# Kernel optimization log

Hardware: AMD Instinct MI355X
Metric: run time of the kernel (lower is better)

Reference implementation:

```python
import jax, jax.numpy as jnp
import numpy as np

D = 128
N = 20000
E = 60000
L = 5  # levels 0..4; level 0 = primary inputs
PER = N // L
# processing order in the original forward: AND(3), NOT(2), XOR(5), MAJ(1), OR(4)
CODES = [3, 2, 5, 1, 4]
FIDX = {3: 0, 5: 1, 1: 2, 4: 3}  # index into 2D-input func aggregators


def _gru(x, h, wih, whh, bih, bhh):
    # single-step torch.nn.GRU cell. wih:[D,3D], whh:[D,3D]
    gi = x @ wih + bih
    gh = h @ whh + bhh
    ir, iz, inn = jnp.split(gi, 3, axis=-1)
    hr, hz, hn = jnp.split(gh, 3, axis=-1)
    r = jax.nn.sigmoid(ir + hr)
    z = jax.nn.sigmoid(iz + hz)
    n = jnp.tanh(inn + r * hn)
    return (1.0 - z) * n + z * h


def setup_inputs() -> dict:
    rng = np.random.default_rng(0)
    # topological levels, contiguous blocks of PER nodes per level
    forward_level = np.repeat(np.arange(L), PER).astype(np.int32)
    gate = np.zeros(N, dtype=np.int32)
    gate[PER:] = rng.integers(1, 6, size=N - PER)  # gates 1..5 for non-PI nodes
    # DAG edges: dst at level>=1, src strictly below dst's level
    dst = rng.integers(PER, N, size=E)
    dst_level = forward_level[dst].astype(np.int64)
    src = (rng.random(E) * (dst_level * PER)).astype(np.int64)
    edge_index = np.stack([src, dst]).astype(np.int32)

    key = jax.random.key(0)
    ks = iter(jax.random.split(key, 64))
    s = 0.08
    p = {}
    p['hs_init'] = jax.random.normal(next(ks), (N, D), jnp.float32)
    # strc aggregators (5 gate types, input D): 2-layer MLP
    p['Ws1'] = jax.random.normal(next(ks), (5, D, D)) * s
    p['bs1'] = jnp.zeros((5, D))
    p['Ws2'] = jax.random.normal(next(ks), (5, D, D)) * s
    p['bs2'] = jnp.zeros((5, D))
    # func aggregators with 2D input (and, xor, maj, or)
    p['Wf1'] = jax.random.normal(next(ks), (4, 2 * D, D)) * s
    p['bf1'] = jnp.zeros((4, D))
    p['Wf2'] = jax.random.normal(next(ks), (4, D, D)) * s
    p['bf2'] = jnp.zeros((4, D))
    # not_func aggregator (input D)
    p['Wnf1'] = jax.random.normal(next(ks), (D, D)) * s
    p['bnf1'] = jnp.zeros((D,))
    p['Wnf2'] = jax.random.normal(next(ks), (D, D)) * s
    p['bnf2'] = jnp.zeros((D,))
    # GRU params, stacked over 5 gate types, strc and func
    for pre in ('Gs', 'Gf'):
        p[pre + '_wih'] = jax.random.normal(next(ks), (5, D, 3 * D)) * s
        p[pre + '_whh'] = jax.random.normal(next(ks), (5, D, 3 * D)) * s
        p[pre + '_bih'] = jnp.zeros((5, 3 * D))
        p[pre + '_bhh'] = jnp.zeros((5, 3 * D))
    p['edge_index'] = jnp.asarray(edge_index)
    p['gate'] = jnp.asarray(gate)
    p['forward_level'] = jnp.asarray(forward_level)
    p['num_levels'] = L
    return p


def reference(hs_init, Ws1, bs1, Ws2, bs2, Wf1, bf1, Wf2, bf2,
              Wnf1, bnf1, Wnf2, bnf2,
              Gs_wih, Gs_whh, Gs_bih, Gs_bhh,
              Gf_wih, Gf_whh, Gf_bih, Gf_bhh,
              edge_index, gate, forward_level, num_levels):
    src, dst = edge_index[0], edge_index[1]
    pi_mask = (gate == 0)
    hs = jnp.where(pi_mask[:, None], hs_init, 0.0)  # generate_hs_init: encode PIs
    hf = jnp.zeros_like(hs)
    node_state = jnp.concatenate([hs, hf], axis=-1)

    for level in range(1, num_levels):
        for t, code in enumerate(CODES):
            nmask = (forward_level == level) & (gate == code)  # [N]
            emask = nmask[dst].astype(hs.dtype)[:, None]       # edges into these nodes
            # --- structural message: MLP(hs[src]) summed into dst
            m = jax.nn.relu(hs[src] @ Ws1[t] + bs1[t]) @ Ws2[t] + bs2[t]
            agg = jax.ops.segment_sum(m * emask, dst, num_segments=N)
            h_new = _gru(agg, hs, Gs_wih[t], Gs_whh[t], Gs_bih[t], Gs_bhh[t])
            hs = jnp.where(nmask[:, None], h_new, hs)
            # --- functional message
            if code == 2:  # NOT uses current hf only
                m = jax.nn.relu(hf[src] @ Wnf1 + bnf1) @ Wnf2 + bnf2
            else:
                fi = FIDX[code]
                m = jax.nn.relu(node_state[src] @ Wf1[fi] + bf1[fi]) @ Wf2[fi] + bf2[fi]
            agg = jax.ops.segment_sum(m * emask, dst, num_segments=N)
            h_new = _gru(agg, hf, Gf_wih[t], Gf_whh[t], Gf_bih[t], Gf_bhh[t])
            hf = jnp.where(nmask[:, None], h_new, hf)
        node_state = jnp.concatenate([hs, hf], axis=-1)
    return hs, hf
```

## Files before the change

kernel.cpp:

```cpp
#include <hip/hip_runtime.h>
#include <hip/hip_bf16.h>

typedef __hip_bfloat16 bf16;
typedef unsigned short ushortT;
typedef __attribute__((ext_vector_type(8))) short bf16x8;
typedef __attribute__((ext_vector_type(4))) float f32x4;

#define D 128
#define NLEV 5
#define TE 16
#define TN 16

#define OFF_S1 0
#define OFF_S2 81920
#define OFF_F1 163840
#define OFF_F2 294912
#define OFF_NF1 360448
#define OFF_NF2 376832
#define WT_TOTAL 393216

__constant__ int TMAP[6] = { -1, 3, 1, 0, 4, 2 };
__constant__ int FMAP[6] = { -1, 2, -1, 0, 3, 1 };

__device__ int g_flag;

__device__ __forceinline__ float sigm(float x) { return 1.0f / (1.0f + __expf(-x)); }

__device__ __forceinline__ float rlane(float v, int ln) {
    return __int_as_float(__builtin_amdgcn_readlane(__float_as_int(v), ln));
}

__device__ __forceinline__ ushortT f2b(float v) {
    bf16 h = __float2bfloat16(v);
    return *reinterpret_cast<ushortT*>(&h);
}

template <int ISB>
__device__ __forceinline__ float ld(const void* p, size_t i) {
    if (ISB) return __bfloat162float(((const bf16*)p)[i]);
    return ((const float*)p)[i];
}

template <int ISB>
__device__ __forceinline__ float2 ld2(const void* p, size_t i) {
    if (ISB) {
        __hip_bfloat162 v = *(const __hip_bfloat162*)((const bf16*)p + i);
        return make_float2(__bfloat162float(v.x), __bfloat162float(v.y));
    }
    return *(const float2*)((const float*)p + i);
}

__global__ void detect_dtype(const void* hs_init) {
    int t = threadIdx.x;
    float x = __bfloat162float(((const bf16*)hs_init)[2 * t]);
    float ax = fabsf(x);
    bool sane = (x == 0.0f) || (ax > 1e-4f && ax < 64.0f);
    unsigned long long m = __ballot(sane);
    if (t == 0) g_flag = (__popcll(m) >= 32) ? 1 : 0;
}

__global__ void init_state(const void* __restrict__ hs_init,
                           const int* __restrict__ gate,
                           float* __restrict__ hs, float* __restrict__ hf,
                           ushortT* __restrict__ hsb, ushortT* __restrict__ hfb) {
    int v = blockIdx.x;
    int j = threadIdx.x;
    size_t idx = (size_t)v * D + j;
    bool pi = (gate[v] == 0);
    float val = 0.f;
    ushortT bval = 0;
    if (pi) {
        if (g_flag) {
            bval = ((const ushortT*)hs_init)[idx];
            bf16 h = *reinterpret_cast<bf16*>(&bval);
            val = __bfloat162float(h);
        } else {
            val = ((const float*)hs_init)[idx];
            bval = f2b(val);
        }
    }
    hs[idx] = val; hf[idx] = 0.f;
    hsb[idx] = bval; hfb[idx] = 0;
}

__global__ void transpose_w(const void* __restrict__ src, ushortT* __restrict__ dst,
                            int K, int C) {
    int n = blockIdx.y, c = blockIdx.x;
    ushortT* d = dst + (size_t)n * C * K;
    if (g_flag) {
        const ushortT* s = (const ushortT*)src + (size_t)n * K * C;
        for (int k = threadIdx.x; k < K; k += blockDim.x)
            d[(size_t)c * K + k] = s[(size_t)k * C + c];
    } else {
        const float* s = (const float*)src + (size_t)n * K * C;
        for (int k = threadIdx.x; k < K; k += blockDim.x)
            d[(size_t)c * K + k] = f2b(s[(size_t)k * C + c]);
    }
}

__global__ void count_bins(const int* __restrict__ dstA, const int* __restrict__ gate,
                           const int* __restrict__ lev, int E, int N,
                           int* __restrict__ ecnt, int* __restrict__ ncnt,
                           int* __restrict__ ndeg) {
    __shared__ int lc[40];
    int tid = threadIdx.x;
    if (tid < 40) lc[tid] = 0;
    __syncthreads();
    int i = blockIdx.x * blockDim.x + tid;
    if (i < E) {
        int d = dstA[i]; int l = lev[d];
        if (l >= 1 && l < NLEV) {
            atomicAdd(&lc[(l - 1) * 5 + TMAP[gate[d]]], 1);
            atomicAdd(&ndeg[d], 1);
        }
    }
    if (i < N) {
        int l = lev[i];
        if (l >= 1 && l < NLEV && gate[i] >= 1) atomicAdd(&lc[20 + (l - 1) * 5 + TMAP[gate[i]]], 1);
    }
    __syncthreads();
    if (tid < 20 && lc[tid]) atomicAdd(&ecnt[tid], lc[tid]);
    if (tid >= 20 && tid < 40 && lc[tid]) atomicAdd(&ncnt[tid - 20], lc[tid]);
}

__global__ void scan_offsets(const int* __restrict__ ecnt, const int* __restrict__ ncnt,
                             int* __restrict__ eoff, int* __restrict__ noff) {
    if (threadIdx.x == 0 && blockIdx.x == 0) {
        int o = 0;
        for (int b = 0; b < 20; ++b) { eoff[b] = o; o += ((ecnt[b] + TE - 1) / TE) * TE; }
        eoff[20] = o;
        o = 0;
        for (int b = 0; b < 20; ++b) { noff[b] = o; o += ((ncnt[b] + TN - 1) / TN) * TN; }
        noff[20] = o;
    }
}

__global__ void fill_bins(const int* __restrict__ gate, const int* __restrict__ lev, int N,
                          const int* __restrict__ noff, int* __restrict__ ncur,
                          int* __restrict__ nlist) {
    __shared__ int nc[20], nb[20];
    int tid = threadIdx.x;
    if (tid < 20) nc[tid] = 0;
    __syncthreads();
    int i = blockIdx.x * blockDim.x + tid;
    int bn = -1, rn = 0;
    if (i < N) {
        int l = lev[i];
        if (l >= 1 && l < NLEV && gate[i] >= 1) { bn = (l - 1) * 5 + TMAP[gate[i]]; rn = atomicAdd(&nc[bn], 1); }
    }
    __syncthreads();
    if (tid < 20) nb[tid] = nc[tid] ? atomicAdd(&ncur[tid], nc[tid]) : 0;
    __syncthreads();
    if (bn >= 0) nlist[noff[bn] + nb[bn] + rn] = i;
}

__global__ __launch_bounds__(256) void bucket_scan(
    const int* __restrict__ nlist, const int* __restrict__ noff,
    const int* __restrict__ ncnt, const int* __restrict__ eoff,
    const int* __restrict__ ndeg, int* __restrict__ nodeoff) {
    int b = blockIdx.x;
    int start = noff[b];
    int cnt = ncnt[b];
    int ebase = eoff[b];
    __shared__ int sc[256];
    int tid = threadIdx.x;
    int carry = 0;
    for (int chunk = 0; chunk < cnt; chunk += 256) {
        __syncthreads();
        int i = chunk + tid;
        int v = -1, dg = 0;
        if (i < cnt) { v = nlist[start + i]; dg = ndeg[v]; }
        sc[tid] = dg;
        __syncthreads();
        for (int off = 1; off < 256; off <<= 1) {
            int y = (tid >= off) ? sc[tid - off] : 0;
            __syncthreads();
            sc[tid] += y;
            __syncthreads();
        }
        if (v >= 0) nodeoff[v] = ebase + carry + (sc[tid] - dg);
        carry += sc[255];
    }
}

__global__ void fill_edges(const int* __restrict__ dstA, const int* __restrict__ lev,
                           int E, const int* __restrict__ nodeoff,
                           int* __restrict__ ecur_n, int* __restrict__ elist) {
    int i = blockIdx.x * blockDim.x + threadIdx.x;
    if (i >= E) return;
    int d = dstA[i];
    int l = lev[d];
    if (l >= 1 && l < NLEV) {
        int pos = nodeoff[d] + atomicAdd(&ecur_n[d], 1);
        elist[pos] = i;
    }
}

__global__ __launch_bounds__(256) void edge_mfma(
    const ushortT* __restrict__ hsb, const ushortT* __restrict__ hfb,
    const ushortT* __restrict__ wt,
    const void* __restrict__ bs1, const void* __restrict__ bs2,
    const void* __restrict__ bf1, const void* __restrict__ bf2,
    const void* __restrict__ bnf1, const void* __restrict__ bnf2,
    const int* __restrict__ dstA, const int* __restrict__ srcA,
    const int* __restrict__ gate,
    const int* __restrict__ eoff, const int* __restrict__ elist,
    float* __restrict__ agg_s, float* __restrict__ agg_f, int level) {
    int lo = eoff[(level - 1) * 5];
    int hi = eoff[(level - 1) * 5 + 5];
    int base = lo + blockIdx.x * TE;
    if (base >= hi) return;

    __shared__ int se[TE], de[TE];
    __shared__ bf16 hid[2][16][136];
    __shared__ float emsg[2][16][128];

    int tid = threadIdx.x;
    int wv = tid >> 6, pass = wv >> 1, hc = wv & 1, l = tid & 63;
    int lg = l >> 4, lr = l & 15;
    int isb = g_flag;

    int c = gate[dstA[elist[base]]];
    int t = TMAP[c], fi = FMAP[c];

    if (tid < TE) {
        int e = elist[base + tid];
        se[tid] = (e < 0) ? -1 : srcA[e];
        de[tid] = (e < 0) ? -1 : dstA[e];
    }
    __syncthreads();

    int src = se[lr];

    int KS1; size_t wb1; int K1;
    if (pass == 0)      { KS1 = 4; wb1 = OFF_S1 + (size_t)t * 16384; K1 = 128; }
    else if (c == 2)    { KS1 = 4; wb1 = OFF_NF1; K1 = 128; }
    else                { KS1 = 8; wb1 = OFF_F1 + (size_t)fi * 32768; K1 = 256; }

    f32x4 a0 = {0.f,0.f,0.f,0.f}, a1 = a0, a2 = a0, a3 = a0;
    for (int ks = 0; ks < KS1; ++ks) {
        bf16x8 a = {0,0,0,0,0,0,0,0};
        if (src >= 0) {
            int kk = ks * 32 + lg * 8;
            const ushortT* ap;
            if (pass == 0)      ap = hsb + (size_t)src * D + kk;
            else if (c == 2)    ap = hfb + (size_t)src * D + kk;
            else                ap = (kk < 128) ? (hsb + (size_t)src * D + kk)
                                                : (hfb + (size_t)src * D + (kk - 128));
            a = *(const bf16x8*)ap;
        }
        int kb = ks * 32 + lg * 8;
        {
            bf16x8 b = *(const bf16x8*)&wt[wb1 + (size_t)(hc * 64 + 0 * 16 + lr) * K1 + kb];
            a0 = __builtin_amdgcn_mfma_f32_16x16x32_bf16(a, b, a0, 0, 0, 0);
        }
        {
            bf16x8 b = *(const bf16x8*)&wt[wb1 + (size_t)(hc * 64 + 1 * 16 + lr) * K1 + kb];
            a1 = __builtin_amdgcn_mfma_f32_16x16x32_bf16(a, b, a1, 0, 0, 0);
        }
        {
            bf16x8 b = *(const bf16x8*)&wt[wb1 + (size_t)(hc * 64 + 2 * 16 + lr) * K1 + kb];
            a2 = __builtin_amdgcn_mfma_f32_16x16x32_bf16(a, b, a2, 0, 0, 0);
        }
        {
            bf16x8 b = *(const bf16x8*)&wt[wb1 + (size_t)(hc * 64 + 3 * 16 + lr) * K1 + kb];
            a3 = __builtin_amdgcn_mfma_f32_16x16x32_bf16(a, b, a3, 0, 0, 0);
        }
    }

    const void* b1p = (pass == 0) ? bs1 : (c == 2 ? bnf1 : bf1);
    size_t b1o = (pass == 0) ? (size_t)t * D : (c == 2 ? 0 : (size_t)fi * D);
    {
        f32x4 av[4] = { a0, a1, a2, a3 };
#pragma unroll
        for (int ct = 0; ct < 4; ++ct) {
            int cc = hc * 64 + ct * 16 + lr;
            float bb = isb ? ld<1>(b1p, b1o + cc) : ld<0>(b1p, b1o + cc);
#pragma unroll
            for (int r = 0; r < 4; ++r) {
                int m = lg * 4 + r;
                float v = fmaxf(av[ct][r] + bb, 0.f);
                hid[pass][m][cc] = __float2bfloat16(v);
            }
        }
    }
    __syncthreads();

    size_t wb2 = (pass == 0) ? (OFF_S2 + (size_t)t * 16384)
                             : (c == 2 ? (size_t)OFF_NF2 : (OFF_F2 + (size_t)fi * 16384));
    a0 = (f32x4){0.f,0.f,0.f,0.f}; a1 = a0; a2 = a0; a3 = a0;
#pragma unroll
    for (int ks = 0; ks < 4; ++ks) {
        bf16x8 a = *(const bf16x8*)&hid[pass][lr][ks * 32 + lg * 8];
        int kb = ks * 32 + lg * 8;
        {
            bf16x8 b = *(const bf16x8*)&wt[wb2 + (size_t)(hc * 64 + 0 * 16 + lr) * 128 + kb];
            a0 = __builtin_amdgcn_mfma_f32_16x16x32_bf16(a, b, a0, 0, 0, 0);
        }
        {
            bf16x8 b = *(const bf16x8*)&wt[wb2 + (size_t)(hc * 64 + 1 * 16 + lr) * 128 + kb];
            a1 = __builtin_amdgcn_mfma_f32_16x16x32_bf16(a, b, a1, 0, 0, 0);
        }
        {
            bf16x8 b = *(const bf16x8*)&wt[wb2 + (size_t)(hc * 64 + 2 * 16 + lr) * 128 + kb];
            a2 = __builtin_amdgcn_mfma_f32_16x16x32_bf16(a, b, a2, 0, 0, 0);
        }
        {
            bf16x8 b = *(const bf16x8*)&wt[wb2 + (size_t)(hc * 64 + 3 * 16 + lr) * 128 + kb];
            a3 = __builtin_amdgcn_mfma_f32_16x16x32_bf16(a, b, a3, 0, 0, 0);
        }
    }

    const void* b2p = (pass == 0) ? bs2 : (c == 2 ? bnf2 : bf2);
    size_t b2o = (pass == 0) ? (size_t)t * D : (c == 2 ? 0 : (size_t)fi * D);
    {
        f32x4 av[4] = { a0, a1, a2, a3 };
#pragma unroll
        for (int ct = 0; ct < 4; ++ct) {
            int cc = hc * 64 + ct * 16 + lr;
            float bb = isb ? ld<1>(b2p, b2o + cc) : ld<0>(b2p, b2o + cc);
#pragma unroll
            for (int r = 0; r < 4; ++r) {
                int m = lg * 4 + r;
                emsg[pass][m][cc] = av[ct][r] + bb;
            }
        }
    }
    __syncthreads();

    float* aggp = pass ? agg_f : agg_s;
    int col = hc * 64 + l;
    float s = 0.f;
    for (int m = 0; m < TE; ++m) {
        int d = de[m];
        if (d < 0) break;
        s += emsg[pass][m][col];
        bool flush = (m == TE - 1) || (de[m + 1] != d);
        if (flush) {
            atomicAdd(&aggp[(size_t)d * D + col], s);
            s = 0.f;
        }
    }
}

template <int ISB, int MC, int R>
__device__ __forceinline__ void mmB(
    const float (&x0)[R], const float (&x1)[R],
    const void* __restrict__ W, size_t wofs, int wstride,
    int mstart, int c0, float (&out)[R][2]) {
#pragma unroll 4
    for (int mm = 0; mm < MC; ++mm) {
        int m = mstart + mm;
        float2 w0 = ld2<ISB>(W, wofs + (size_t)(2 * m) * wstride + c0);
        float2 w1 = ld2<ISB>(W, wofs + (size_t)(2 * m + 1) * wstride + c0);
#pragma unroll
        for (int r = 0; r < R; ++r) {
            float xa = rlane(x0[r], m);
            float xb = rlane(x1[r], m);
            out[r][0] = fmaf(xb, w1.x, fmaf(xa, w0.x, out[r][0]));
            out[r][1] = fmaf(xb, w1.y, fmaf(xa, w0.y, out[r][1]));
        }
    }
}

template <int ISB>
__device__ void node_fused_body(
    const float* __restrict__ agg_s, const float* __restrict__ agg_f,
    const void* __restrict__ Gs_wih, const void* __restrict__ Gf_wih,
    const void* __restrict__ Gs_bih, const void* __restrict__ Gs_bhh,
    const void* __restrict__ Gf_bih, const void* __restrict__ Gf_bhh,
    float* __restrict__ hs, float* __restrict__ hf,
    ushortT* __restrict__ hsb, ushortT* __restrict__ hfb,
    const int* __restrict__ gate,
    const int* __restrict__ noff, const int* __restrict__ nlist,
    int level, float (*gi)[3][16][128]) {
    int lo = noff[(level - 1) * 5];
    int hi = noff[(level - 1) * 5 + 5];
    int base = lo + blockIdx.x * TN;
    if (base >= hi) return;
    int tid = threadIdx.x;
    int w = tid >> 6, l = tid & 63;
    int p = w / 6, r6 = w % 6, gg = r6 >> 1, rh = r6 & 1;
    int c0 = 2 * l;
    int t = TMAP[gate[nlist[base]]];

    const float* agg = p ? agg_f : agg_s;
    const void* wih = p ? Gf_wih : Gs_wih;

    float x0[8], x1[8];
#pragma unroll
    for (int r = 0; r < 8; ++r) {
        int v = nlist[base + rh * 8 + r];
        float2 a = (v >= 0) ? *(const float2*)&agg[(size_t)v * D + c0]
                            : make_float2(0.f, 0.f);
        x0[r] = a.x; x1[r] = a.y;
    }
    float acc[8][2];
#pragma unroll
    for (int r = 0; r < 8; ++r) { acc[r][0] = 0.f; acc[r][1] = 0.f; }
    mmB<ISB, 64, 8>(x0, x1, wih, (size_t)t * D * 3 * D, 3 * D, 0, gg * 128 + c0, acc);
#pragma unroll
    for (int r = 0; r < 8; ++r) {
        gi[p][gg][rh * 8 + r][c0] = acc[r][0];
        gi[p][gg][rh * 8 + r][c0 + 1] = acc[r][1];
    }
    __syncthreads();

    if (tid < 256) {
        int pp = tid >> 7, j = tid & 127;
        const void* bih = pp ? Gf_bih : Gs_bih;
        const void* bhh = pp ? Gf_bhh : Gs_bhh;
        float br = ld<ISB>(bih, (size_t)t * 384 + j);
        float bz = ld<ISB>(bih, (size_t)t * 384 + 128 + j);
        float bn = ld<ISB>(bih, (size_t)t * 384 + 256 + j);
        float hr = ld<ISB>(bhh, (size_t)t * 384 + j);
        float hz = ld<ISB>(bhh, (size_t)t * 384 + 128 + j);
        float hn = ld<ISB>(bhh, (size_t)t * 384 + 256 + j);
        float* ho = pp ? hf : hs;
        ushortT* hb = pp ? hfb : hsb;
#pragma unroll
        for (int r = 0; r < TN; ++r) {
            int v = nlist[base + r];
            if (v < 0) continue;
            float rr = sigm(gi[pp][0][r][j] + br + hr);
            float z = sigm(gi[pp][1][r][j] + bz + hz);
            float n = tanhf(gi[pp][2][r][j] + bn + rr * hn);
            float out = (1.f - z) * n;
            ho[(size_t)v * D + j] = out;
            hb[(size_t)v * D + j] = f2b(out);
        }
    }
}

__global__ __launch_bounds__(768) void node_fused(
    const float* agg_s, const float* agg_f,
    const void* Gs_wih, const void* Gf_wih,
    const void* Gs_bih, const void* Gs_bhh,
    const void* Gf_bih, const void* Gf_bhh,
    float* hs, float* hf, ushortT* hsb, ushortT* hfb,
    const int* gate, const int* noff, const int* nlist, int level) {
    __shared__ float gi[2][3][16][128];
    if (g_flag)
        node_fused_body<1>(agg_s, agg_f, Gs_wih, Gf_wih, Gs_bih, Gs_bhh,
                           Gf_bih, Gf_bhh, hs, hf, hsb, hfb, gate, noff, nlist,
                           level, gi);
    else
        node_fused_body<0>(agg_s, agg_f, Gs_wih, Gf_wih, Gs_bih, Gs_bhh,
                           Gf_bih, Gf_bhh, hs, hf, hsb, hfb, gate, noff, nlist,
                           level, gi);
}

__global__ void writeout(const float* __restrict__ hs, const float* __restrict__ hf,
                         void* __restrict__ out, int ND) {
    int i = blockIdx.x * blockDim.x + threadIdx.x;
    if (i >= ND) return;
    if (g_flag) {
        ((ushortT*)out)[i] = f2b(hs[i]);
        ((ushortT*)out)[ND + i] = f2b(hf[i]);
    } else {
        ((float*)out)[i] = hs[i];
        ((float*)out)[ND + i] = hf[i];
    }
}

extern "C" void kernel_launch(void* const* d_in, const int* in_sizes, int n_in,
                              void* d_out, int out_size, void* d_ws, size_t ws_size,
                              hipStream_t stream) {
    const void* hs_init = d_in[0];
    const void* Ws1 = d_in[1];
    const void* bs1 = d_in[2];
    const void* Ws2 = d_in[3];
    const void* bs2 = d_in[4];
    const void* Wf1 = d_in[5];
    const void* bf1 = d_in[6];
    const void* Wf2 = d_in[7];
    const void* bf2 = d_in[8];
    const void* Wnf1 = d_in[9];
    const void* bnf1 = d_in[10];
    const void* Wnf2 = d_in[11];
    const void* bnf2 = d_in[12];
    const void* Gs_wih = d_in[13];
    const void* Gs_bih = d_in[15];
    const void* Gs_bhh = d_in[16];
    const void* Gf_wih = d_in[17];
    const void* Gf_bih = d_in[19];
    const void* Gf_bhh = d_in[20];
    const int* edge_index = (const int*)d_in[21];
    const int* gate = (const int*)d_in[22];
    const int* lev = (const int*)d_in[23];

    int E = in_sizes[21] / 2;
    int N = in_sizes[22];
    int ND = N * D;
    int cap = ((N / NLEV + 5 * TN + 64) + TN - 1) / TN * TN;

    float* hs = (float*)d_ws;
    float* hf = hs + ND;
    float* agg_s = hf + ND;
    float* agg_f = agg_s + ND;
    ushortT* hsb = (ushortT*)(agg_f + ND);
    ushortT* hfb = hsb + ND;
    ushortT* wt = hfb + ND;
    int* meta = (int*)(wt + WT_TOTAL);
    int* ecnt = meta;
    int* ncnt = ecnt + 20;
    int* ncur = ncnt + 20;
    int* eoff = ncur + 20;
    int* noff = eoff + 21;
    int* ndeg = meta + 128;
    int* ecur_n = ndeg + N;
    int* nodeoff = ecur_n + N;
    int* elist = nodeoff + N;
    int* nlist = elist + (E + 20 * TE);

    const int* srcA = edge_index;
    const int* dstA = edge_index + E;

    detect_dtype<<<1, 64, 0, stream>>>(hs_init);
    hipMemsetAsync(agg_s, 0, (size_t)2 * ND * sizeof(float), stream);
    hipMemsetAsync(meta, 0, (size_t)(128 + 2 * N) * sizeof(int), stream);
    hipMemsetAsync(elist, 0xFF, (size_t)(E + 20 * TE + N + 20 * TN) * sizeof(int), stream);
    init_state<<<N, D, 0, stream>>>(hs_init, gate, hs, hf, hsb, hfb);

    transpose_w<<<dim3(128, 5), 128, 0, stream>>>(Ws1, wt + OFF_S1, 128, 128);
    transpose_w<<<dim3(128, 5), 128, 0, stream>>>(Ws2, wt + OFF_S2, 128, 128);
    transpose_w<<<dim3(128, 4), 256, 0, stream>>>(Wf1, wt + OFF_F1, 256, 128);
    transpose_w<<<dim3(128, 4), 128, 0, stream>>>(Wf2, wt + OFF_F2, 128, 128);
    transpose_w<<<dim3(128, 1), 128, 0, stream>>>(Wnf1, wt + OFF_NF1, 128, 128);
    transpose_w<<<dim3(128, 1), 128, 0, stream>>>(Wnf2, wt + OFF_NF2, 128, 128);

    int mx = (E > N) ? E : N;
    count_bins<<<(mx + 255) / 256, 256, 0, stream>>>(dstA, gate, lev, E, N, ecnt, ncnt, ndeg);
    scan_offsets<<<1, 64, 0, stream>>>(ecnt, ncnt, eoff, noff);
    fill_bins<<<(N + 255) / 256, 256, 0, stream>>>(gate, lev, N, noff, ncur, nlist);
    bucket_scan<<<20, 256, 0, stream>>>(nlist, noff, ncnt, eoff, ndeg, nodeoff);
    fill_edges<<<(E + 255) / 256, 256, 0, stream>>>(dstA, lev, E, nodeoff, ecur_n, elist);

    int gridE = (E + 20 * TE) / TE + 1;
    int gridNcap = cap / TN;
    for (int level = 1; level < NLEV; ++level) {
        edge_mfma<<<gridE, 256, 0, stream>>>(hsb, hfb, wt,
                                             bs1, bs2, bf1, bf2, bnf1, bnf2,
                                             dstA, srcA, gate, eoff, elist,
                                             agg_s, agg_f, level);
        node_fused<<<gridNcap, 768, 0, stream>>>(agg_s, agg_f, Gs_wih, Gf_wih,
                                                 Gs_bih, Gs_bhh, Gf_bih, Gf_bhh,
                                                 hs, hf, hsb, hfb,
                                                 gate, noff, nlist, level);
    }

    writeout<<<(ND + 255) / 256, 256, 0, stream>>>(hs, hf, d_out, ND);
}
```

Baseline: 302.2 us.

## Use split-bf16 MFMA for node GRU input projection with pretransposed weights

Replaces the scalar readlane/FMA matmul for the GRU input projection in node_fused with bf16 MFMA 16x16x32 instructions. To keep accuracy close to fp32, activations are split into hi and lo bf16 parts, and for fp32 inputs the weights get a lo residual too (three MFMAs per tile). GRU weights are pretransposed to bf16 hi/lo buffers in a single merged prep_weights kernel that replaces six transpose launches. This adds workspace and extra MFMA passes, and the split-bf16 scheme is not exactly equal to fp32 accumulation.

```diff
diff --git a/kernel.cpp b/kernel.cpp
--- a/kernel.cpp
+++ b/kernel.cpp
@@ -17,7 +17,11 @@
 #define OFF_F2 294912
 #define OFF_NF1 360448
 #define OFF_NF2 376832
-#define WT_TOTAL 393216
+#define OFF_GSH 393216
+#define OFF_GFH 638976
+#define OFF_GSL 884736
+#define OFF_GFL 1130496
+#define WT_TOTAL 1376256
 
 __constant__ int TMAP[6] = { -1, 3, 1, 0, 4, 2 };
 __constant__ int FMAP[6] = { -1, 2, -1, 0, 3, 1 };
@@ -25,10 +29,6 @@
 __device__ int g_flag;
 
 __device__ __forceinline__ float sigm(float x) { return 1.0f / (1.0f + __expf(-x)); }
-
-__device__ __forceinline__ float rlane(float v, int ln) {
-    return __int_as_float(__builtin_amdgcn_readlane(__float_as_int(v), ln));
-}
 
 __device__ __forceinline__ ushortT f2b(float v) {
     bf16 h = __float2bfloat16(v);
@@ -39,15 +39,6 @@
 __device__ __forceinline__ float ld(const void* p, size_t i) {
     if (ISB) return __bfloat162float(((const bf16*)p)[i]);
     return ((const float*)p)[i];
-}
-
-template <int ISB>
-__device__ __forceinline__ float2 ld2(const void* p, size_t i) {
-    if (ISB) {
-        __hip_bfloat162 v = *(const __hip_bfloat162*)((const bf16*)p + i);
-        return make_float2(__bfloat162float(v.x), __bfloat162float(v.y));
-    }
-    return *(const float2*)((const float*)p + i);
 }
 
 __global__ void detect_dtype(const void* hs_init) {
@@ -83,19 +74,38 @@
     hsb[idx] = bval; hfb[idx] = 0;
 }
 
-__global__ void transpose_w(const void* __restrict__ src, ushortT* __restrict__ dst,
-                            int K, int C) {
-    int n = blockIdx.y, c = blockIdx.x;
-    ushortT* d = dst + (size_t)n * C * K;
-    if (g_flag) {
-        const ushortT* s = (const ushortT*)src + (size_t)n * K * C;
-        for (int k = threadIdx.x; k < K; k += blockDim.x)
-            d[(size_t)c * K + k] = s[(size_t)k * C + c];
+__global__ void prep_weights(const void* __restrict__ Ws1, const void* __restrict__ Ws2,
+                             const void* __restrict__ Wf1, const void* __restrict__ Wf2,
+                             const void* __restrict__ Wnf1, const void* __restrict__ Wnf2,
+                             const void* __restrict__ Gs, const void* __restrict__ Gf,
+                             ushortT* __restrict__ wt) {
+    int i = blockIdx.x * blockDim.x + threadIdx.x;
+    if (i >= WT_TOTAL) return;
+    const void* src; int Kd, C, rem, mode = 0;
+    if (i < OFF_S2)       { src = Ws1;  rem = i;           Kd = 128; C = 128; }
+    else if (i < OFF_F1)  { src = Ws2;  rem = i - OFF_S2;  Kd = 128; C = 128; }
+    else if (i < OFF_F2)  { src = Wf1;  rem = i - OFF_F1;  Kd = 256; C = 128; }
+    else if (i < OFF_NF1) { src = Wf2;  rem = i - OFF_F2;  Kd = 128; C = 128; }
+    else if (i < OFF_NF2) { src = Wnf1; rem = i - OFF_NF1; Kd = 128; C = 128; }
+    else if (i < OFF_GSH) { src = Wnf2; rem = i - OFF_NF2; Kd = 128; C = 128; }
+    else if (i < OFF_GFH) { src = Gs;   rem = i - OFF_GSH; Kd = 128; C = 384; mode = 1; }
+    else if (i < OFF_GSL) { src = Gf;   rem = i - OFF_GFH; Kd = 128; C = 384; mode = 1; }
+    else if (i < OFF_GFL) { src = Gs;   rem = i - OFF_GSL; Kd = 128; C = 384; mode = 2; }
+    else                  { src = Gf;   rem = i - OFF_GFL; Kd = 128; C = 384; mode = 2; }
+    int n = rem / (Kd * C);
+    int r2 = rem % (Kd * C);
+    int c = r2 / Kd;
+    int k = r2 % Kd;
+    size_t si = (size_t)n * Kd * C + (size_t)k * C + c;
+    float v = g_flag ? ld<1>(src, si) : ld<0>(src, si);
+    ushortT out;
+    if (mode == 2) {
+        bf16 h = __float2bfloat16(v);
+        out = f2b(v - __bfloat162float(h));
     } else {
-        const float* s = (const float*)src + (size_t)n * K * C;
-        for (int k = threadIdx.x; k < K; k += blockDim.x)
-            d[(size_t)c * K + k] = f2b(s[(size_t)k * C + c]);
-    }
+        out = f2b(v);
+    }
+    wt[i] = out;
 }
 
 __global__ void count_bins(const int* __restrict__ dstA, const int* __restrict__ gate,
@@ -343,30 +353,10 @@
     }
 }
 
-template <int ISB, int MC, int R>
-__device__ __forceinline__ void mmB(
-    const float (&x0)[R], const float (&x1)[R],
-    const void* __restrict__ W, size_t wofs, int wstride,
-    int mstart, int c0, float (&out)[R][2]) {
-#pragma unroll 4
-    for (int mm = 0; mm < MC; ++mm) {
-        int m = mstart + mm;
-        float2 w0 = ld2<ISB>(W, wofs + (size_t)(2 * m) * wstride + c0);
-        float2 w1 = ld2<ISB>(W, wofs + (size_t)(2 * m + 1) * wstride + c0);
-#pragma unroll
-        for (int r = 0; r < R; ++r) {
-            float xa = rlane(x0[r], m);
-            float xb = rlane(x1[r], m);
-            out[r][0] = fmaf(xb, w1.x, fmaf(xa, w0.x, out[r][0]));
-            out[r][1] = fmaf(xb, w1.y, fmaf(xa, w0.y, out[r][1]));
-        }
-    }
-}
-
 template <int ISB>
 __device__ void node_fused_body(
     const float* __restrict__ agg_s, const float* __restrict__ agg_f,
-    const void* __restrict__ Gs_wih, const void* __restrict__ Gf_wih,
+    const ushortT* __restrict__ wt,
     const void* __restrict__ Gs_bih, const void* __restrict__ Gs_bhh,
     const void* __restrict__ Gf_bih, const void* __restrict__ Gf_bhh,
     float* __restrict__ hs, float* __restrict__ hf,
@@ -380,29 +370,56 @@
     if (base >= hi) return;
     int tid = threadIdx.x;
     int w = tid >> 6, l = tid & 63;
-    int p = w / 6, r6 = w % 6, gg = r6 >> 1, rh = r6 & 1;
-    int c0 = 2 * l;
+    int lg = l >> 4, lr = l & 15;
+    int p = w / 6, cg = w % 6;
     int t = TMAP[gate[nlist[base]]];
 
     const float* agg = p ? agg_f : agg_s;
-    const void* wih = p ? Gf_wih : Gs_wih;
-
-    float x0[8], x1[8];
-#pragma unroll
-    for (int r = 0; r < 8; ++r) {
-        int v = nlist[base + rh * 8 + r];
-        float2 a = (v >= 0) ? *(const float2*)&agg[(size_t)v * D + c0]
-                            : make_float2(0.f, 0.f);
-        x0[r] = a.x; x1[r] = a.y;
-    }
-    float acc[8][2];
-#pragma unroll
-    for (int r = 0; r < 8; ++r) { acc[r][0] = 0.f; acc[r][1] = 0.f; }
-    mmB<ISB, 64, 8>(x0, x1, wih, (size_t)t * D * 3 * D, 3 * D, 0, gg * 128 + c0, acc);
-#pragma unroll
-    for (int r = 0; r < 8; ++r) {
-        gi[p][gg][rh * 8 + r][c0] = acc[r][0];
-        gi[p][gg][rh * 8 + r][c0 + 1] = acc[r][1];
+    size_t wbh = (p ? OFF_GFH : OFF_GSH) + (size_t)t * 49152;
+    size_t wbl = (p ? OFF_GFL : OFF_GSL) + (size_t)t * 49152;
+
+    int v = nlist[base + lr];
+
+    f32x4 acc[4];
+#pragma unroll
+    for (int q = 0; q < 4; ++q) acc[q] = (f32x4){0.f, 0.f, 0.f, 0.f};
+
+    for (int ks = 0; ks < 4; ++ks) {
+        bf16x8 ahi = {0,0,0,0,0,0,0,0}, alo = ahi;
+        if (v >= 0) {
+            const float* ap = agg + (size_t)v * D + ks * 32 + lg * 8;
+            float4 f0 = *(const float4*)ap;
+            float4 f1 = *(const float4*)(ap + 4);
+            float av[8] = { f0.x, f0.y, f0.z, f0.w, f1.x, f1.y, f1.z, f1.w };
+#pragma unroll
+            for (int j = 0; j < 8; ++j) {
+                bf16 h = __float2bfloat16(av[j]);
+                ahi[j] = (short)*reinterpret_cast<ushortT*>(&h);
+                float r = av[j] - __bfloat162float(h);
+                bf16 l2 = __float2bfloat16(r);
+                alo[j] = (short)*reinterpret_cast<ushortT*>(&l2);
+            }
+        }
+        int kb = ks * 32 + lg * 8;
+#pragma unroll
+        for (int q = 0; q < 4; ++q) {
+            int col = (cg * 4 + q) * 16 + lr;
+            bf16x8 bh = *(const bf16x8*)&wt[wbh + (size_t)col * 128 + kb];
+            acc[q] = __builtin_amdgcn_mfma_f32_16x16x32_bf16(ahi, bh, acc[q], 0, 0, 0);
+            acc[q] = __builtin_amdgcn_mfma_f32_16x16x32_bf16(alo, bh, acc[q], 0, 0, 0);
+            if (!ISB) {
+                bf16x8 bl = *(const bf16x8*)&wt[wbl + (size_t)col * 128 + kb];
+                acc[q] = __builtin_amdgcn_mfma_f32_16x16x32_bf16(ahi, bl, acc[q], 0, 0, 0);
+            }
+        }
+    }
+
+#pragma unroll
+    for (int q = 0; q < 4; ++q) {
+        int ct = cg * 4 + q;
+        int g = ct >> 3, j = (ct & 7) * 16 + lr;
+#pragma unroll
+        for (int r = 0; r < 4; ++r) gi[p][g][lg * 4 + r][j] = acc[q][r];
     }
     __syncthreads();
 
@@ -420,34 +437,31 @@
         ushortT* hb = pp ? hfb : hsb;
 #pragma unroll
         for (int r = 0; r < TN; ++r) {
-            int v = nlist[base + r];
-            if (v < 0) continue;
+            int vv = nlist[base + r];
+            if (vv < 0) continue;
             float rr = sigm(gi[pp][0][r][j] + br + hr);
             float z = sigm(gi[pp][1][r][j] + bz + hz);
             float n = tanhf(gi[pp][2][r][j] + bn + rr * hn);
             float out = (1.f - z) * n;
-            ho[(size_t)v * D + j] = out;
-            hb[(size_t)v * D + j] = f2b(out);
+            ho[(size_t)vv * D + j] = out;
+            hb[(size_t)vv * D + j] = f2b(out);
         }
     }
 }
 
 __global__ __launch_bounds__(768) void node_fused(
-    const float* agg_s, const float* agg_f,
-    const void* Gs_wih, const void* Gf_wih,
+    const float* agg_s, const float* agg_f, const ushortT* wt,
     const void* Gs_bih, const void* Gs_bhh,
     const void* Gf_bih, const void* Gf_bhh,
     float* hs, float* hf, ushortT* hsb, ushortT* hfb,
     const int* gate, const int* noff, const int* nlist, int level) {
     __shared__ float gi[2][3][16][128];
     if (g_flag)
-        node_fused_body<1>(agg_s, agg_f, Gs_wih, Gf_wih, Gs_bih, Gs_bhh,
-                           Gf_bih, Gf_bhh, hs, hf, hsb, hfb, gate, noff, nlist,
-                           level, gi);
+        node_fused_body<1>(agg_s, agg_f, wt, Gs_bih, Gs_bhh, Gf_bih, Gf_bhh,
+                           hs, hf, hsb, hfb, gate, noff, nlist, level, gi);
     else
-        node_fused_body<0>(agg_s, agg_f, Gs_wih, Gf_wih, Gs_bih, Gs_bhh,
-                           Gf_bih, Gf_bhh, hs, hf, hsb, hfb, gate, noff, nlist,
-                           level, gi);
+        node_fused_body<0>(agg_s, agg_f, wt, Gs_bih, Gs_bhh, Gf_bih, Gf_bhh,
+                           hs, hf, hsb, hfb, gate, noff, nlist, level, gi);
 }
 
 __global__ void writeout(const float* __restrict__ hs, const float* __restrict__ hf,
@@ -522,12 +536,8 @@
     hipMemsetAsync(elist, 0xFF, (size_t)(E + 20 * TE + N + 20 * TN) * sizeof(int), stream);
     init_state<<<N, D, 0, stream>>>(hs_init, gate, hs, hf, hsb, hfb);
 
-    transpose_w<<<dim3(128, 5), 128, 0, stream>>>(Ws1, wt + OFF_S1, 128, 128);
-    transpose_w<<<dim3(128, 5), 128, 0, stream>>>(Ws2, wt + OFF_S2, 128, 128);
-    transpose_w<<<dim3(128, 4), 256, 0, stream>>>(Wf1, wt + OFF_F1, 256, 128);
-    transpose_w<<<dim3(128, 4), 128, 0, stream>>>(Wf2, wt + OFF_F2, 128, 128);
-    transpose_w<<<dim3(128, 1), 128, 0, stream>>>(Wnf1, wt + OFF_NF1, 128, 128);
-    transpose_w<<<dim3(128, 1), 128, 0, stream>>>(Wnf2, wt + OFF_NF2, 128, 128);
+    prep_weights<<<(WT_TOTAL + 255) / 256, 256, 0, stream>>>(
+        Ws1, Ws2, Wf1, Wf2, Wnf1, Wnf2, Gs_wih, Gf_wih, wt);
 
     int mx = (E > N) ? E : N;
     count_bins<<<(mx + 255) / 256, 256, 0, stream>>>(dstA, gate, lev, E, N, ecnt, ncnt, ndeg);
@@ -543,7 +553,7 @@
                                              bs1, bs2, bf1, bf2, bnf1, bnf2,
                                              dstA, srcA, gate, eoff, elist,
                                              agg_s, agg_f, level);
-        node_fused<<<gridNcap, 768, 0, stream>>>(agg_s, agg_f, Gs_wih, Gf_wih,
+        node_fused<<<gridNcap, 768, 0, stream>>>(agg_s, agg_f, wt,
                                                  Gs_bih, Gs_bhh, Gf_bih, Gf_bhh,
                                                  hs, hf, hsb, hfb,
                                                  gate, noff, nlist, level);
```

Result: faster. 267.5 us (-11.5%).
